# Kernel tuning notes

Measured on AMD Instinct MI355X. Metric: run time of the kernel, lower is better.

The kernel has to match this reference:

```python
import jax, jax.numpy as jnp
import numpy as np

EPS = 1e-8  # torch nn.CosineSimilarity default eps


def setup_inputs() -> dict:
    key = jax.random.key(0)
    k1, k2 = jax.random.split(key)
    query = jax.random.normal(k1, (8, 2048, 64), dtype=jnp.float32)
    y = jax.random.normal(k2, (8, 2048, 64), dtype=jnp.float32)
    return {"query": query, "y": y}


def _l2_normalize(x):
    # x / max(||x||, eps) along last dim (matches torch cosine_similarity clamping)
    n = jnp.sqrt(jnp.sum(x * x, axis=-1, keepdims=True))
    return x / jnp.maximum(n, EPS)


def reference(query, y):
    # Algebraically equivalent to broadcast CosineSimilarity over [B,Lq,Ly,D]:
    # normalize once, then batched GEMM -> [B, Lq, Ly]
    qn = _l2_normalize(query)          # [B, Lq, D]
    yn = _l2_normalize(y)              # [B, Ly, D]
    att = jnp.einsum("bqd,bkd->bqk", qn, yn)  # [B, Lq, Ly]
    sim = jnp.max(att, axis=2)[:, None, :]     # [B, 1, Lq]
    return (att, sim)
```

## Files before the change

### kernel.cpp

```cpp
#include <hip/hip_runtime.h>

#define LL 2048
#define DD 64
#define BB 8
#define EPSF 1e-8f

#define NELEM ((size_t)BB * LL * DD)

typedef short bf16x8 __attribute__((ext_vector_type(8)));
typedef float f32x4 __attribute__((ext_vector_type(4)));

__device__ __forceinline__ ushort f2bf(float f) {
    uint u = __float_as_uint(f);
    return (ushort)((u + 0x7fffu + ((u >> 16) & 1u)) >> 16);
}
__device__ __forceinline__ float bf2f(ushort h) {
    return __uint_as_float((uint)h << 16);
}

__global__ __launch_bounds__(256) void norm_split_kernel(
    const float* __restrict__ q, const float* __restrict__ y,
    ushort* __restrict__ ws) {
    const int row   = blockIdx.x * 32 + (threadIdx.x >> 3);
    const int oct   = threadIdx.x & 7;
    const int which = blockIdx.y;
    const float* src = which ? y : q;
    ushort* hi = ws + (size_t)which * NELEM;
    ushort* lo = ws + 2 * NELEM + (size_t)which * NELEM;

    const float* g = src + (size_t)row * DD;
    float4 v0 = *reinterpret_cast<const float4*>(g + oct * 4);
    float4 v1 = *reinterpret_cast<const float4*>(g + 32 + oct * 4);
    float ss = v0.x*v0.x + v0.y*v0.y + v0.z*v0.z + v0.w*v0.w
             + v1.x*v1.x + v1.y*v1.y + v1.z*v1.z + v1.w*v1.w;
    ss += __shfl_xor(ss, 1);
    ss += __shfl_xor(ss, 2);
    ss += __shfl_xor(ss, 4);
    const float sc = 1.0f / fmaxf(sqrtf(ss), EPSF);

    const float f[8] = {v0.x*sc, v0.y*sc, v0.z*sc, v0.w*sc,
                        v1.x*sc, v1.y*sc, v1.z*sc, v1.w*sc};
    ushort h[8], l8[8];
    #pragma unroll
    for (int i = 0; i < 8; ++i) {
        h[i]  = f2bf(f[i]);
        l8[i] = f2bf(f[i] - bf2f(h[i]));
    }
    const size_t base = (size_t)row * DD + oct * 4;
    *reinterpret_cast<ushort4*>(hi + base)      = make_ushort4(h[0], h[1], h[2], h[3]);
    *reinterpret_cast<ushort4*>(hi + base + 32) = make_ushort4(h[4], h[5], h[6], h[7]);
    *reinterpret_cast<ushort4*>(lo + base)      = make_ushort4(l8[0], l8[1], l8[2], l8[3]);
    *reinterpret_cast<ushort4*>(lo + base + 32) = make_ushort4(l8[4], l8[5], l8[6], l8[7]);
}

__global__ __launch_bounds__(256, 2) void att_mfma_kernel(
    const ushort* __restrict__ ws, float* __restrict__ out) {
    const int b       = blockIdx.y;
    const int rowBase = blockIdx.x * 32;
    const int t  = threadIdx.x;
    const int w  = t >> 6;
    const int l  = t & 63;
    const int ln = l & 15;
    const int kg = l >> 4;

    const ushort* qh = ws;
    const ushort* yh = ws + NELEM;
    const ushort* ql = ws + 2 * NELEM;
    const ushort* yl = ws + 3 * NELEM;

    bf16x8 qhf[2][2], qlf[2][2];
    #pragma unroll
    for (int mq = 0; mq < 2; ++mq)
        #pragma unroll
        for (int kk = 0; kk < 2; ++kk) {
            const size_t off =
                ((size_t)(b * LL + rowBase + mq * 16 + ln)) * DD + kk * 32 + kg * 8;
            qhf[mq][kk] = *reinterpret_cast<const bf16x8*>(qh + off);
            qlf[mq][kk] = *reinterpret_cast<const bf16x8*>(ql + off);
        }

    float rmax[2] = {-1e30f, -1e30f};

    bf16x8 yh0[4][2], yl0[4][2], yh1[4][2], yl1[4][2];

#define LOADY(DH, DL, CT) do {                                                   \
    const int colBase_ = (CT) * 256 + w * 64;                                    \
    _Pragma("unroll")                                                            \
    for (int ny = 0; ny < 4; ++ny) {                                             \
        _Pragma("unroll")                                                        \
        for (int kk = 0; kk < 2; ++kk) {                                         \
            const size_t off_ =                                                  \
                ((size_t)(b * LL + colBase_ + ny * 16 + ln)) * DD + kk * 32 + kg * 8; \
            DH[ny][kk] = *reinterpret_cast<const bf16x8*>(yh + off_);            \
            DL[ny][kk] = *reinterpret_cast<const bf16x8*>(yl + off_);            \
        }                                                                        \
    }                                                                            \
} while (0)

#define COMPSTORE(SH, SL, CT) do {                                               \
    const int colBase_ = (CT) * 256 + w * 64;                                    \
    f32x4 acc[2][4];                                                             \
    _Pragma("unroll")                                                            \
    for (int mq = 0; mq < 2; ++mq)                                               \
        _Pragma("unroll")                                                        \
        for (int ny = 0; ny < 4; ++ny)                                           \
            acc[mq][ny] = (f32x4){0.f, 0.f, 0.f, 0.f};                           \
    _Pragma("unroll")                                                            \
    for (int kk = 0; kk < 2; ++kk)                                               \
        _Pragma("unroll")                                                        \
        for (int mq = 0; mq < 2; ++mq)                                           \
            _Pragma("unroll")                                                    \
            for (int ny = 0; ny < 4; ++ny)                                       \
                acc[mq][ny] = __builtin_amdgcn_mfma_f32_16x16x32_bf16(           \
                    SL[ny][kk], qhf[mq][kk], acc[mq][ny], 0, 0, 0);              \
    _Pragma("unroll")                                                            \
    for (int kk = 0; kk < 2; ++kk)                                               \
        _Pragma("unroll")                                                        \
        for (int mq = 0; mq < 2; ++mq)                                           \
            _Pragma("unroll")                                                    \
            for (int ny = 0; ny < 4; ++ny)                                       \
                acc[mq][ny] = __builtin_amdgcn_mfma_f32_16x16x32_bf16(           \
                    SH[ny][kk], qlf[mq][kk], acc[mq][ny], 0, 0, 0);              \
    _Pragma("unroll")                                                            \
    for (int kk = 0; kk < 2; ++kk)                                               \
        _Pragma("unroll")                                                        \
        for (int mq = 0; mq < 2; ++mq)                                           \
            _Pragma("unroll")                                                    \
            for (int ny = 0; ny < 4; ++ny)                                       \
                acc[mq][ny] = __builtin_amdgcn_mfma_f32_16x16x32_bf16(           \
                    SH[ny][kk], qhf[mq][kk], acc[mq][ny], 0, 0, 0);              \
    _Pragma("unroll")                                                            \
    for (int mq = 0; mq < 2; ++mq) {                                             \
        _Pragma("unroll")                                                        \
        for (int ny = 0; ny < 4; ++ny) {                                         \
            f32x4 v = acc[mq][ny];                                               \
            *reinterpret_cast<f32x4*>(                                           \
                out + ((size_t)(b * LL + rowBase + mq * 16 + ln)) * LL           \
                    + colBase_ + ny * 16 + kg * 4) = v;                          \
            rmax[mq] = fmaxf(rmax[mq],                                           \
                       fmaxf(fmaxf(v[0], v[1]), fmaxf(v[2], v[3])));             \
        }                                                                        \
    }                                                                            \
} while (0)

    LOADY(yh0, yl0, 0);
    #pragma unroll
    for (int ct = 0; ct < 8; ct += 2) {
        if (ct + 1 < 8) LOADY(yh1, yl1, ct + 1);
        COMPSTORE(yh0, yl0, ct);
        if (ct + 2 < 8) LOADY(yh0, yl0, ct + 2);
        if (ct + 1 < 8) COMPSTORE(yh1, yl1, ct + 1);
    }

    #pragma unroll
    for (int mq = 0; mq < 2; ++mq) {
        rmax[mq] = fmaxf(rmax[mq], __shfl_xor(rmax[mq], 16));
        rmax[mq] = fmaxf(rmax[mq], __shfl_xor(rmax[mq], 32));
    }

    __shared__ float smax[4][32];
    if (kg == 0) {
        smax[w][ln]      = rmax[0];
        smax[w][16 + ln] = rmax[1];
    }
    __syncthreads();
    if (t < 32) {
        const float v = fmaxf(fmaxf(smax[0][t], smax[1][t]),
                              fmaxf(smax[2][t], smax[3][t]));
        out[(size_t)BB * LL * LL + (size_t)b * LL + rowBase + t] = v;
    }
#undef LOADY
#undef COMPSTORE
}

extern "C" void kernel_launch(void* const* d_in, const int* in_sizes, int n_in,
                              void* d_out, int out_size, void* d_ws, size_t ws_size,
                              hipStream_t stream) {
    const float* q = (const float*)d_in[0];
    const float* y = (const float*)d_in[1];
    float* out     = (float*)d_out;
    ushort* ws     = (ushort*)d_ws;

    norm_split_kernel<<<dim3(512, 2), dim3(256), 0, stream>>>(q, y, ws);
    att_mfma_kernel<<<dim3(LL / 32, BB), dim3(256), 0, stream>>>(ws, out);
}
```

Baseline: 164.4 us.

## Drop y low-part split, fuse q normalization into MFMA kernel

```diff
diff --git a/kernel.cpp b/kernel.cpp
--- a/kernel.cpp
+++ b/kernel.cpp
@@ -9,6 +9,7 @@
 
 typedef short bf16x8 __attribute__((ext_vector_type(8)));
 typedef float f32x4 __attribute__((ext_vector_type(4)));
+typedef float f32x8 __attribute__((ext_vector_type(8)));
 
 __device__ __forceinline__ ushort f2bf(float f) {
     uint u = __float_as_uint(f);
@@ -18,17 +19,11 @@
     return __uint_as_float((uint)h << 16);
 }
 
-__global__ __launch_bounds__(256) void norm_split_kernel(
-    const float* __restrict__ q, const float* __restrict__ y,
-    ushort* __restrict__ ws) {
-    const int row   = blockIdx.x * 32 + (threadIdx.x >> 3);
-    const int oct   = threadIdx.x & 7;
-    const int which = blockIdx.y;
-    const float* src = which ? y : q;
-    ushort* hi = ws + (size_t)which * NELEM;
-    ushort* lo = ws + 2 * NELEM + (size_t)which * NELEM;
-
-    const float* g = src + (size_t)row * DD;
+__global__ __launch_bounds__(256) void norm_y_kernel(
+    const float* __restrict__ y, ushort* __restrict__ yh) {
+    const int row = blockIdx.x * 32 + (threadIdx.x >> 3);
+    const int oct = threadIdx.x & 7;
+    const float* g = y + (size_t)row * DD;
     float4 v0 = *reinterpret_cast<const float4*>(g + oct * 4);
     float4 v1 = *reinterpret_cast<const float4*>(g + 32 + oct * 4);
     float ss = v0.x*v0.x + v0.y*v0.y + v0.z*v0.z + v0.w*v0.w
@@ -37,24 +32,16 @@
     ss += __shfl_xor(ss, 2);
     ss += __shfl_xor(ss, 4);
     const float sc = 1.0f / fmaxf(sqrtf(ss), EPSF);
-
-    const float f[8] = {v0.x*sc, v0.y*sc, v0.z*sc, v0.w*sc,
-                        v1.x*sc, v1.y*sc, v1.z*sc, v1.w*sc};
-    ushort h[8], l8[8];
-    #pragma unroll
-    for (int i = 0; i < 8; ++i) {
-        h[i]  = f2bf(f[i]);
-        l8[i] = f2bf(f[i] - bf2f(h[i]));
-    }
     const size_t base = (size_t)row * DD + oct * 4;
-    *reinterpret_cast<ushort4*>(hi + base)      = make_ushort4(h[0], h[1], h[2], h[3]);
-    *reinterpret_cast<ushort4*>(hi + base + 32) = make_ushort4(h[4], h[5], h[6], h[7]);
-    *reinterpret_cast<ushort4*>(lo + base)      = make_ushort4(l8[0], l8[1], l8[2], l8[3]);
-    *reinterpret_cast<ushort4*>(lo + base + 32) = make_ushort4(l8[4], l8[5], l8[6], l8[7]);
+    *reinterpret_cast<ushort4*>(yh + base) =
+        make_ushort4(f2bf(v0.x*sc), f2bf(v0.y*sc), f2bf(v0.z*sc), f2bf(v0.w*sc));
+    *reinterpret_cast<ushort4*>(yh + base + 32) =
+        make_ushort4(f2bf(v1.x*sc), f2bf(v1.y*sc), f2bf(v1.z*sc), f2bf(v1.w*sc));
 }
 
-__global__ __launch_bounds__(256, 2) void att_mfma_kernel(
-    const ushort* __restrict__ ws, float* __restrict__ out) {
+__global__ __launch_bounds__(256, 3) void att_mfma_kernel(
+    const float* __restrict__ q, const ushort* __restrict__ yhg,
+    float* __restrict__ out) {
     const int b       = blockIdx.y;
     const int rowBase = blockIdx.x * 32;
     const int t  = threadIdx.x;
@@ -63,41 +50,49 @@
     const int ln = l & 15;
     const int kg = l >> 4;
 
-    const ushort* qh = ws;
-    const ushort* yh = ws + NELEM;
-    const ushort* ql = ws + 2 * NELEM;
-    const ushort* yl = ws + 3 * NELEM;
-
     bf16x8 qhf[2][2], qlf[2][2];
     #pragma unroll
-    for (int mq = 0; mq < 2; ++mq)
+    for (int mq = 0; mq < 2; ++mq) {
+        f32x8 v[2];
         #pragma unroll
-        for (int kk = 0; kk < 2; ++kk) {
-            const size_t off =
-                ((size_t)(b * LL + rowBase + mq * 16 + ln)) * DD + kk * 32 + kg * 8;
-            qhf[mq][kk] = *reinterpret_cast<const bf16x8*>(qh + off);
-            qlf[mq][kk] = *reinterpret_cast<const bf16x8*>(ql + off);
-        }
+        for (int kk = 0; kk < 2; ++kk)
+            v[kk] = *reinterpret_cast<const f32x8*>(
+                q + ((size_t)(b * LL + rowBase + mq * 16 + ln)) * DD + kk * 32 + kg * 8);
+        float ss = 0.f;
+        #pragma unroll
+        for (int kk = 0; kk < 2; ++kk)
+            #pragma unroll
+            for (int j = 0; j < 8; ++j) ss += v[kk][j] * v[kk][j];
+        ss += __shfl_xor(ss, 16);
+        ss += __shfl_xor(ss, 32);
+        const float sc = 1.0f / fmaxf(sqrtf(ss), EPSF);
+        #pragma unroll
+        for (int kk = 0; kk < 2; ++kk)
+            #pragma unroll
+            for (int j = 0; j < 8; ++j) {
+                const float f = v[kk][j] * sc;
+                const ushort h = f2bf(f);
+                qhf[mq][kk][j] = (short)h;
+                qlf[mq][kk][j] = (short)f2bf(f - bf2f(h));
+            }
+    }
 
     float rmax[2] = {-1e30f, -1e30f};
 
-    bf16x8 yh0[4][2], yl0[4][2], yh1[4][2], yl1[4][2];
+    bf16x8 yh0[4][2], yh1[4][2];
 
-#define LOADY(DH, DL, CT) do {                                                   \
+#define LOADY(DH, CT) do {                                                       \
     const int colBase_ = (CT) * 256 + w * 64;                                    \
     _Pragma("unroll")                                                            \
-    for (int ny = 0; ny < 4; ++ny) {                                             \
+    for (int ny = 0; ny < 4; ++ny)                                               \
         _Pragma("unroll")                                                        \
-        for (int kk = 0; kk < 2; ++kk) {                                         \
-            const size_t off_ =                                                  \
-                ((size_t)(b * LL + colBase_ + ny * 16 + ln)) * DD + kk * 32 + kg * 8; \
-            DH[ny][kk] = *reinterpret_cast<const bf16x8*>(yh + off_);            \
-            DL[ny][kk] = *reinterpret_cast<const bf16x8*>(yl + off_);            \
-        }                                                                        \
-    }                                                                            \
+        for (int kk = 0; kk < 2; ++kk)                                           \
+            DH[ny][kk] = *reinterpret_cast<const bf16x8*>(                       \
+                yhg + ((size_t)(b * LL + colBase_ + ny * 16 + ln)) * DD          \
+                    + kk * 32 + kg * 8);                                         \
 } while (0)
 
-#define COMPSTORE(SH, SL, CT) do {                                               \
+#define COMPSTORE(SH, CT) do {                                                   \
     const int colBase_ = (CT) * 256 + w * 64;                                    \
     f32x4 acc[2][4];                                                             \
     _Pragma("unroll")                                                            \
@@ -105,14 +100,6 @@
         _Pragma("unroll")                                                        \
         for (int ny = 0; ny < 4; ++ny)                                           \
             acc[mq][ny] = (f32x4){0.f, 0.f, 0.f, 0.f};                           \
-    _Pragma("unroll")                                                            \
-    for (int kk = 0; kk < 2; ++kk)                                               \
-        _Pragma("unroll")                                                        \
-        for (int mq = 0; mq < 2; ++mq)                                           \
-            _Pragma("unroll")                                                    \
-            for (int ny = 0; ny < 4; ++ny)                                       \
-                acc[mq][ny] = __builtin_amdgcn_mfma_f32_16x16x32_bf16(           \
-                    SL[ny][kk], qhf[mq][kk], acc[mq][ny], 0, 0, 0);              \
     _Pragma("unroll")                                                            \
     for (int kk = 0; kk < 2; ++kk)                                               \
         _Pragma("unroll")                                                        \
@@ -143,13 +130,13 @@
     }                                                                            \
 } while (0)
 
-    LOADY(yh0, yl0, 0);
+    LOADY(yh0, 0);
     #pragma unroll
     for (int ct = 0; ct < 8; ct += 2) {
-        if (ct + 1 < 8) LOADY(yh1, yl1, ct + 1);
-        COMPSTORE(yh0, yl0, ct);
-        if (ct + 2 < 8) LOADY(yh0, yl0, ct + 2);
-        if (ct + 1 < 8) COMPSTORE(yh1, yl1, ct + 1);
+        if (ct + 1 < 8) LOADY(yh1, ct + 1);
+        COMPSTORE(yh0, ct);
+        if (ct + 2 < 8) LOADY(yh0, ct + 2);
+        if (ct + 1 < 8) COMPSTORE(yh1, ct + 1);
     }
 
     #pragma unroll
@@ -179,8 +166,8 @@
     const float* q = (const float*)d_in[0];
     const float* y = (const float*)d_in[1];
     float* out     = (float*)d_out;
-    ushort* ws     = (ushort*)d_ws;
+    ushort* yh     = (ushort*)d_ws;
 
-    norm_split_kernel<<<dim3(512, 2), dim3(256), 0, stream>>>(q, y, ws);
-    att_mfma_kernel<<<dim3(LL / 32, BB), dim3(256), 0, stream>>>(ws, out);
+    norm_y_kernel<<<dim3(512), dim3(256), 0, stream>>>(y, yh);
+    att_mfma_kernel<<<dim3(LL / 32, BB), dim3(256), 0, stream>>>(q, yh, out);
 }
```

Result: faster. 150.4 us (-8.5%).
